# Kernel optimization log

Hardware: AMD Instinct MI355X
Metric: run time of the kernel (lower is better)

Reference implementation:

```python
import jax, jax.numpy as jnp
import numpy as np

LMAX, MMAX = 6, 2
N_NODES, N_EDGES = 10000, 80000
C_SPH = 32            # sphere_channels
D_DIST, H = 128, 64   # distance-basis width, radial hidden
MAX_ELEM = 90
RESCALE = 5.862
NUM_COEF_FULL = (LMAX + 1) ** 2   # 49
M0 = LMAX + 1                     # m=0 coefficient count = 7

def _orders():
    # reduced l-primary ordering: (l, m) for l in 0..LMAX, |m| <= min(l, MMAX)
    lp = [(l, m) for l in range(LMAX + 1) for m in range(-min(l, MMAX), min(l, MMAX) + 1)]
    # reduced m-primary ordering: m=0 block first, then (+m, -m) blocks, l ascending
    mp = [(l, 0) for l in range(LMAX + 1)]
    for m in range(1, MMAX + 1):
        mp += [(l, m) for l in range(m, LMAX + 1)]
        mp += [(l, -m) for l in range(m, LMAX + 1)]
    perm = np.array([mp.index(t) for t in lp])  # gather: m-primary -> l-primary
    full = [(l, m) for l in range(LMAX + 1) for m in range(-l, l + 1)]
    mask = np.array([i for i, (l, m) in enumerate(full) if abs(m) <= MMAX])
    return perm, mask

PERM_M2L, WIG_MASK = _orders()
M_ALL = len(PERM_M2L)  # 29


def setup_inputs() -> dict:
    key = jax.random.key(0)
    ks = jax.random.split(key, 10)
    return {
        "atomic_numbers": jax.random.randint(ks[0], (N_NODES,), 0, MAX_ELEM),
        "edge_index": jax.random.randint(ks[1], (2, N_EDGES), 0, N_NODES),
        "edge_distance": jax.random.normal(ks[2], (N_EDGES, D_DIST), jnp.float32),
        "wigner_inv": jax.random.normal(ks[3], (N_EDGES, NUM_COEF_FULL, NUM_COEF_FULL), jnp.float32) / np.float32(NUM_COEF_FULL) ** 0.5,
        "src_emb": jax.random.uniform(ks[4], (MAX_ELEM, H), jnp.float32, -0.001, 0.001),
        "tgt_emb": jax.random.uniform(ks[5], (MAX_ELEM, H), jnp.float32, -0.001, 0.001),
        "W1": jax.random.normal(ks[6], (D_DIST + 2 * H, H), jnp.float32) / np.float32(D_DIST + 2 * H) ** 0.5,
        "b1": jnp.zeros((H,), jnp.float32),
        "g1": jnp.ones((H,), jnp.float32),
        "be1": jnp.zeros((H,), jnp.float32),
        "W2": jax.random.normal(ks[7], (H, H), jnp.float32) / np.float32(H) ** 0.5,
        "b2": jnp.zeros((H,), jnp.float32),
        "g2": jnp.ones((H,), jnp.float32),
        "be2": jnp.zeros((H,), jnp.float32),
        "W3": jax.random.normal(ks[8], (H, M0 * C_SPH), jnp.float32) / np.float32(H) ** 0.5,
        "b3": jnp.zeros((M0 * C_SPH,), jnp.float32),
    }


def _ln(x, g, b):
    mu = jnp.mean(x, axis=-1, keepdims=True)
    var = jnp.var(x, axis=-1, keepdims=True)
    return (x - mu) * jax.lax.rsqrt(var + 1e-5) * g + b


def reference(atomic_numbers, edge_index, edge_distance, wigner_inv,
              src_emb, tgt_emb, W1, b1, g1, be1, W2, b2, g2, be2, W3, b3):
    # gather per-edge atom embeddings and build invariant edge scalars
    src = src_emb[atomic_numbers[edge_index[0]]]          # [E, H]
    tgt = tgt_emb[atomic_numbers[edge_index[1]]]          # [E, H]
    x = jnp.concatenate([edge_distance, src, tgt], axis=1)  # [E, D0+2H]
    # RadialFunction: Linear+LN+SiLU x2, final Linear -> m0 * C
    x = jax.nn.silu(_ln(x @ W1 + b1, g1, be1))
    x = jax.nn.silu(_ln(x @ W2 + b2, g2, be2))
    x = (x @ W3 + b3).reshape(-1, M0, C_SPH)              # [E, 7, C], m=0 coefficients
    # pad the m != 0 coefficients with zeros (m-primary layout, m=0 first)
    x = jnp.pad(x, ((0, 0), (0, M_ALL - M0), (0, 0)))     # [E, 29, C]
    # _l_primary: permute m-primary -> l-primary (to_m is a permutation matrix)
    x = x[:, PERM_M2L]                                    # [E, 29, C]
    # _rotate_inv: per-edge Wigner-D inverse, columns restricted to |m| <= mmax
    x = jnp.einsum('eij,ejc->eic', wigner_inv[:, :, WIG_MASK], x)  # [E, 49, C]
    # _reduce_edge: scatter-sum messages onto target nodes
    out = jax.ops.segment_sum(x, edge_index[1], num_segments=N_NODES)  # [N, 49, C]
    return out / RESCALE
```

## Files before the change

### kernel.cpp

```cpp
#include <hip/hip_runtime.h>
#include <hip/hip_bf16.h>
#include <stdint.h>

#define E_EDGES 80000
#define N_NODES 10000
#define HD      64
#define DDIST   128
#define NCOEF   49
#define W3OUT   224
#define WROW    2401
#define NELEM   90

typedef float  f32x4  __attribute__((ext_vector_type(4)));
typedef short  bf16x8 __attribute__((ext_vector_type(8)));
typedef unsigned int  uint_t;
typedef unsigned short ushort_t;

__device__ __forceinline__ ushort_t f2b(float f) {
    uint_t u = __builtin_bit_cast(uint_t, f);
    return (ushort_t)((u + 0x7FFFu + ((u >> 16) & 1u)) >> 16);
}
__device__ __forceinline__ uint_t pack2(float a, float b) {
    return (uint_t)f2b(a) | ((uint_t)f2b(b) << 16);
}

__global__ __launch_bounds__(256) void k_prep(
    const float* __restrict__ semb, const float* __restrict__ temb,
    const float* __restrict__ W1, const float* __restrict__ W2,
    const float* __restrict__ W3,
    float* __restrict__ sW1, float* __restrict__ tW1,
    ushort_t* __restrict__ W1T, ushort_t* __restrict__ W2T,
    ushort_t* __restrict__ W3T, int* __restrict__ cnt)
{
    const int gid = blockIdx.x * 256 + threadIdx.x;
    if (gid < NELEM * 64) {
        const int z = gid >> 6, n = gid & 63;
        float sa = 0.f, ta = 0.f;
        #pragma unroll 4
        for (int k = 0; k < 64; k++) {
            sa = fmaf(semb[z * 64 + k], W1[(128 + k) * 64 + n], sa);
            ta = fmaf(temb[z * 64 + k], W1[(192 + k) * 64 + n], ta);
        }
        sW1[z * 64 + n] = sa;
        tW1[z * 64 + n] = ta;
    }
    if (gid < 8192)  { const int n = gid >> 7, k = gid & 127; W1T[gid] = f2b(W1[k * 64 + n]); }
    if (gid < 4096)  { const int n = gid >> 6, k = gid & 63;  W2T[gid] = f2b(W2[k * 64 + n]); }
    if (gid < 14336) { const int n = gid >> 6, k = gid & 63;  W3T[gid] = f2b(W3[k * W3OUT + n]); }
    if (gid < N_NODES) cnt[gid] = 0;
}

__global__ __launch_bounds__(256, 3) void k_mlp(
    const int* __restrict__ an, const int* __restrict__ ei,
    const float* __restrict__ ed,
    const float* __restrict__ sW1, const float* __restrict__ tW1,
    const ushort_t* __restrict__ W1T, const ushort_t* __restrict__ W2T,
    const ushort_t* __restrict__ W3T,
    const float* __restrict__ b1, const float* __restrict__ g1,
    const float* __restrict__ be1,
    const float* __restrict__ b2, const float* __restrict__ g2,
    const float* __restrict__ be2,
    const float* __restrict__ b3, float* __restrict__ y3)
{
    __shared__ __align__(16) ushort_t Xs[64 * 128];
    __shared__ __align__(16) ushort_t Ws[64 * 128];
    __shared__ __align__(16) ushort_t Hs[64 * 64];
    __shared__ __align__(16) ushort_t H2s[64 * 64];

    const int tid  = threadIdx.x;
    const int wave = tid >> 6, lane = tid & 63;
    const int e0   = blockIdx.x * 64;
    const int mo   = wave * 16;
    const int cl   = lane & 15;
    const int kgr  = lane >> 4;

    {
        const int m = tid >> 2, q = tid & 3;
        const float4* ed4 = (const float4*)(ed + (size_t)(e0 + m) * DDIST);
        #pragma unroll
        for (int j = 0; j < 4; j++) {
            const int kb = q * 4 + j;
            const float4 f0 = ed4[kb * 2];
            const float4 f1 = ed4[kb * 2 + 1];
            uint4 p;
            p.x = pack2(f0.x, f0.y); p.y = pack2(f0.z, f0.w);
            p.z = pack2(f1.x, f1.y); p.w = pack2(f1.z, f1.w);
            *(uint4*)&Xs[m * 128 + ((kb ^ (m & 15)) * 8)] = p;
        }
    }
    {
        const uint4* src = (const uint4*)W1T;
        #pragma unroll
        for (int i = 0; i < 4; i++) {
            const int B = tid + i * 256;
            const int n = B >> 4, kb = B & 15;
            *(uint4*)&Ws[n * 128 + ((kb ^ (n & 15)) * 8)] = src[B];
        }
    }

    f32x4 acc[4];
    {
        const int er0 = e0 + mo + kgr * 4;
        const int4 s4 = *(const int4*)&ei[er0];
        const int4 t4 = *(const int4*)&ei[E_EDGES + er0];
        const int zs0 = an[s4.x], zs1 = an[s4.y], zs2 = an[s4.z], zs3 = an[s4.w];
        const int zt0 = an[t4.x], zt1 = an[t4.y], zt2 = an[t4.z], zt3 = an[t4.w];
        #pragma unroll
        for (int nf = 0; nf < 4; nf++) {
            const int col = nf * 16 + cl;
            acc[nf][0] = sW1[zs0 * 64 + col] + tW1[zt0 * 64 + col];
            acc[nf][1] = sW1[zs1 * 64 + col] + tW1[zt1 * 64 + col];
            acc[nf][2] = sW1[zs2 * 64 + col] + tW1[zt2 * 64 + col];
            acc[nf][3] = sW1[zs3 * 64 + col] + tW1[zt3 * 64 + col];
        }
    }
    __syncthreads();

    {
        const int m = mo + cl;
        #pragma unroll
        for (int kc = 0; kc < 4; kc++) {
            const int kb = kc * 4 + kgr;
            const bf16x8 a = *(const bf16x8*)&Xs[m * 128 + ((kb ^ (m & 15)) * 8)];
            #pragma unroll
            for (int nf = 0; nf < 4; nf++) {
                const int n = nf * 16 + cl;
                const bf16x8 b = *(const bf16x8*)&Ws[n * 128 + ((kb ^ (n & 15)) * 8)];
                acc[nf] = __builtin_amdgcn_mfma_f32_16x16x32_bf16(a, b, acc[nf], 0, 0, 0);
            }
        }
    }

    {
        float b1v[4], g1v[4], e1v[4];
        #pragma unroll
        for (int nf = 0; nf < 4; nf++) {
            b1v[nf] = b1[nf * 16 + cl];
            g1v[nf] = g1[nf * 16 + cl];
            e1v[nf] = be1[nf * 16 + cl];
        }
        #pragma unroll
        for (int nf = 0; nf < 4; nf++)
            #pragma unroll
            for (int r = 0; r < 4; r++) acc[nf][r] += b1v[nf];
        #pragma unroll
        for (int r = 0; r < 4; r++) {
            float s = acc[0][r] + acc[1][r] + acc[2][r] + acc[3][r];
            float q = acc[0][r]*acc[0][r] + acc[1][r]*acc[1][r]
                    + acc[2][r]*acc[2][r] + acc[3][r]*acc[3][r];
            s += __shfl_xor(s, 1, 64); q += __shfl_xor(q, 1, 64);
            s += __shfl_xor(s, 2, 64); q += __shfl_xor(q, 2, 64);
            s += __shfl_xor(s, 4, 64); q += __shfl_xor(q, 4, 64);
            s += __shfl_xor(s, 8, 64); q += __shfl_xor(q, 8, 64);
            const float mu  = s * (1.f / 64.f);
            const float var = fmaxf(q * (1.f / 64.f) - mu * mu, 0.f);
            const float rstd = rsqrtf(var + 1e-5f);
            const int m_h = mo + kgr * 4 + r;
            #pragma unroll
            for (int nf = 0; nf < 4; nf++) {
                const float t = (acc[nf][r] - mu) * rstd * g1v[nf] + e1v[nf];
                const float h = t / (1.f + expf(-t));
                const int ch = nf * 16 + cl;
                Hs[m_h * 64 + (((ch >> 3) ^ (m_h & 7)) * 8) + (ch & 7)] = f2b(h);
            }
        }
    }
    __syncthreads();

    {
        const uint4* src = (const uint4*)W2T;
        #pragma unroll
        for (int i = 0; i < 2; i++) {
            const int B = tid + i * 256;
            const int n = B >> 3, kb = B & 7;
            *(uint4*)&Ws[n * 64 + ((kb ^ (n & 7)) * 8)] = src[B];
        }
    }
    __syncthreads();

    f32x4 acc2[4];
    {
        const f32x4 z = {0.f, 0.f, 0.f, 0.f};
        acc2[0] = z; acc2[1] = z; acc2[2] = z; acc2[3] = z;
        const int m = mo + cl;
        #pragma unroll
        for (int kc = 0; kc < 2; kc++) {
            const int kb = kc * 4 + kgr;
            const bf16x8 a = *(const bf16x8*)&Hs[m * 64 + ((kb ^ (m & 7)) * 8)];
            #pragma unroll
            for (int nf = 0; nf < 4; nf++) {
                const int n = nf * 16 + cl;
                const bf16x8 b = *(const bf16x8*)&Ws[n * 64 + ((kb ^ (n & 7)) * 8)];
                acc2[nf] = __builtin_amdgcn_mfma_f32_16x16x32_bf16(a, b, acc2[nf], 0, 0, 0);
            }
        }
    }

    {
        float b2v[4], g2v[4], e2v[4];
        #pragma unroll
        for (int nf = 0; nf < 4; nf++) {
            b2v[nf] = b2[nf * 16 + cl];
            g2v[nf] = g2[nf * 16 + cl];
            e2v[nf] = be2[nf * 16 + cl];
        }
        #pragma unroll
        for (int nf = 0; nf < 4; nf++)
            #pragma unroll
            for (int r = 0; r < 4; r++) acc2[nf][r] += b2v[nf];
        #pragma unroll
        for (int r = 0; r < 4; r++) {
            float s = acc2[0][r] + acc2[1][r] + acc2[2][r] + acc2[3][r];
            float q = acc2[0][r]*acc2[0][r] + acc2[1][r]*acc2[1][r]
                    + acc2[2][r]*acc2[2][r] + acc2[3][r]*acc2[3][r];
            s += __shfl_xor(s, 1, 64); q += __shfl_xor(q, 1, 64);
            s += __shfl_xor(s, 2, 64); q += __shfl_xor(q, 2, 64);
            s += __shfl_xor(s, 4, 64); q += __shfl_xor(q, 4, 64);
            s += __shfl_xor(s, 8, 64); q += __shfl_xor(q, 8, 64);
            const float mu  = s * (1.f / 64.f);
            const float var = fmaxf(q * (1.f / 64.f) - mu * mu, 0.f);
            const float rstd = rsqrtf(var + 1e-5f);
            const int m_h = mo + kgr * 4 + r;
            #pragma unroll
            for (int nf = 0; nf < 4; nf++) {
                const float t = (acc2[nf][r] - mu) * rstd * g2v[nf] + e2v[nf];
                const float h = t / (1.f + expf(-t));
                const int ch = nf * 16 + cl;
                H2s[m_h * 64 + (((ch >> 3) ^ (m_h & 7)) * 8) + (ch & 7)] = f2b(h);
            }
        }
    }
    __syncthreads();

    const int er0 = e0 + mo + kgr * 4;
    #pragma unroll
    for (int half = 0; half < 2; half++) {
        {
            const uint4* src = (const uint4*)W3T;
            #pragma unroll
            for (int i = 0; i < 4; i++) {
                const int B = tid + i * 256;
                if (B < 896) {
                    const int nn = B >> 3, kb = B & 7;
                    *(uint4*)&Ws[nn * 64 + ((kb ^ (nn & 7)) * 8)] = src[half * 896 + B];
                }
            }
        }
        __syncthreads();

        f32x4 acc3[7];
        {
            const f32x4 z = {0.f, 0.f, 0.f, 0.f};
            #pragma unroll
            for (int nf = 0; nf < 7; nf++) acc3[nf] = z;
        }
        const int m = mo + cl;
        #pragma unroll
        for (int kc = 0; kc < 2; kc++) {
            const int kb = kc * 4 + kgr;
            const bf16x8 a = *(const bf16x8*)&H2s[m * 64 + ((kb ^ (m & 7)) * 8)];
            #pragma unroll
            for (int nf = 0; nf < 7; nf++) {
                const int nn = nf * 16 + cl;
                const bf16x8 b = *(const bf16x8*)&Ws[nn * 64 + ((kb ^ (nn & 7)) * 8)];
                acc3[nf] = __builtin_amdgcn_mfma_f32_16x16x32_bf16(a, b, acc3[nf], 0, 0, 0);
            }
        }
        #pragma unroll
        for (int nf = 0; nf < 7; nf++) {
            const int ch = half * 112 + nf * 16 + cl;
            const float bv = b3[ch];
            #pragma unroll
            for (int r = 0; r < 4; r++)
                y3[(size_t)(er0 + r) * W3OUT + ch] =
                    (acc3[nf][r] + bv) * (1.0f / 5.862f);
        }
        __syncthreads();
    }
}

__global__ void k_count(const int* __restrict__ ei, int* __restrict__ cnt) {
    const int e = blockIdx.x * 256 + threadIdx.x;
    if (e < E_EDGES) atomicAdd(&cnt[ei[E_EDGES + e]], 1);
}

__global__ __launch_bounds__(1024) void k_scan(const int* __restrict__ cnt,
                                               int* __restrict__ offs,
                                               int* __restrict__ cursor) {
    __shared__ int wsum[16];
    __shared__ int carry_s;
    const int tid  = threadIdx.x;
    const int lane = tid & 63;
    const int wid  = tid >> 6;
    if (tid == 0) carry_s = 0;
    __syncthreads();
    for (int base = 0; base < N_NODES; base += 1024) {
        const int idx = base + tid;
        const int v = (idx < N_NODES) ? cnt[idx] : 0;
        int s = v;
        #pragma unroll
        for (int off = 1; off < 64; off <<= 1) {
            const int t = __shfl_up(s, off, 64);
            if (lane >= off) s += t;
        }
        if (lane == 63) wsum[wid] = s;
        __syncthreads();
        if (wid == 0) {
            const int t = (lane < 16) ? wsum[lane] : 0;
            int ss = t;
            #pragma unroll
            for (int off = 1; off < 16; off <<= 1) {
                const int u = __shfl_up(ss, off, 64);
                if (lane >= off) ss += u;
            }
            if (lane < 16) wsum[lane] = ss - t;
        }
        __syncthreads();
        const int carry = carry_s;
        const int excl = carry + wsum[wid] + s - v;
        if (idx < N_NODES) { offs[idx] = excl; cursor[idx] = excl; }
        __syncthreads();
        if (tid == 1023) carry_s = carry + wsum[15] + s;
    }
    __syncthreads();
    if (tid == 0) offs[N_NODES] = carry_s;
}

__global__ void k_scatter(const int* __restrict__ ei, int* __restrict__ cursor,
                          int* __restrict__ eids) {
    const int e = blockIdx.x * 256 + threadIdx.x;
    if (e < E_EDGES) {
        const int pos = atomicAdd(&cursor[ei[E_EDGES + e]], 1);
        eids[pos] = e;
    }
}

__global__ __launch_bounds__(256) void k_out(
    const float* __restrict__ wig, const float* __restrict__ y3,
    const int* __restrict__ offs, const int* __restrict__ eids,
    float* __restrict__ out)
{
    __shared__ __align__(16) float wl[4][2][400];
    __shared__ __align__(16) float yl[4][2][224];
    const int tid  = threadIdx.x;
    const int wave = tid >> 6;
    const int lane = tid & 63;
    const int n    = blockIdx.x * 4 + wave;
    const int c    = lane & 31;
    const int h    = lane >> 5;
    const int beg  = offs[n];
    const int end  = offs[n + 1];

    float acc[25];
    #pragma unroll
    for (int r = 0; r < 25; r++) acc[r] = 0.f;

    float gv[6];
    float4 yv;

    #define GATHER(E) do {                                                  \
        const float* __restrict__ wb_ = wig + (size_t)(E) * WROW;           \
        _Pragma("unroll")                                                   \
        for (int g = 0; g < 6; g++) {                                       \
            const int t = lane + 64 * g;                                    \
            if (t < 343) {                                                  \
                const int row = t / 7;                                      \
                const int l   = t - row * 7;                                \
                gv[g] = wb_[row * 49 + l * l + l];                          \
            }                                                               \
        }                                                                   \
        if (lane < 56)                                                      \
            yv = ((const float4*)(y3 + (size_t)(E) * W3OUT))[lane];         \
    } while (0)

    #define COMMIT(B) do {                                                  \
        _Pragma("unroll")                                                   \
        for (int g = 0; g < 6; g++) {                                       \
            const int t = lane + 64 * g;                                    \
            if (t < 343) {                                                  \
                const int row = t / 7;                                      \
                const int l   = t - row * 7;                                \
                wl[wave][B][row * 8 + l] = gv[g];                           \
            }                                                               \
        }                                                                   \
        if (lane < 56) ((float4*)yl[wave][B])[lane] = yv;                   \
    } while (0)

    if (beg < end) {
        GATHER(eids[beg]);
        COMMIT(0);
    }

    int cur = 0;
    for (int ie = beg; ie < end; ie++) {
        if (ie + 1 < end) GATHER(eids[ie + 1]);
        asm volatile("s_waitcnt lgkmcnt(0)" ::: "memory");
        __builtin_amdgcn_sched_barrier(0);

        float yr[7];
        #pragma unroll
        for (int l = 0; l < 7; l++) yr[l] = yl[wave][cur][l * 32 + c];
        #pragma unroll
        for (int r = 0; r < 25; r++) {
            const int i = 2 * r + h;
            if (i < NCOEF) {
                const float4 wa = *(const float4*)(&wl[wave][cur][i * 8]);
                const float4 wb = *(const float4*)(&wl[wave][cur][i * 8 + 4]);
                acc[r] += wa.x * yr[0] + wa.y * yr[1] + wa.z * yr[2] + wa.w * yr[3]
                        + wb.x * yr[4] + wb.y * yr[5] + wb.z * yr[6];
            }
        }
        if (ie + 1 < end) COMMIT(cur ^ 1);
        cur ^= 1;
    }

    #pragma unroll
    for (int r = 0; r < 25; r++) {
        const int i = 2 * r + h;
        if (i < NCOEF)
            out[(size_t)n * (NCOEF * 32) + i * 32 + c] = acc[r];
    }
}

extern "C" void kernel_launch(void* const* d_in, const int* in_sizes, int n_in,
                              void* d_out, int out_size, void* d_ws, size_t ws_size,
                              hipStream_t stream)
{
    const int*   an   = (const int*)  d_in[0];
    const int*   ei   = (const int*)  d_in[1];
    const float* ed   = (const float*)d_in[2];
    const float* wig  = (const float*)d_in[3];
    const float* semb = (const float*)d_in[4];
    const float* temb = (const float*)d_in[5];
    const float* W1   = (const float*)d_in[6];
    const float* b1   = (const float*)d_in[7];
    const float* g1   = (const float*)d_in[8];
    const float* be1  = (const float*)d_in[9];
    const float* W2   = (const float*)d_in[10];
    const float* b2   = (const float*)d_in[11];
    const float* g2   = (const float*)d_in[12];
    const float* be2  = (const float*)d_in[13];
    const float* W3   = (const float*)d_in[14];
    const float* b3   = (const float*)d_in[15];
    float* out = (float*)d_out;

    uintptr_t p = (uintptr_t)d_ws;
    #define ALLOC(ptr, type, count) \
        p = (p + 15) & ~(uintptr_t)15; type* ptr = (type*)p; p += sizeof(type) * (count)
    ALLOC(y3,     float,    (size_t)E_EDGES * W3OUT);
    ALLOC(cnt,    int,      N_NODES);
    ALLOC(offs,   int,      N_NODES + 1);
    ALLOC(cursor, int,      N_NODES);
    ALLOC(eids,   int,      E_EDGES);
    ALLOC(sW1,    float,    NELEM * HD);
    ALLOC(tW1,    float,    NELEM * HD);
    ALLOC(W1T,    ushort_t, 64 * 128);
    ALLOC(W2T,    ushort_t, 64 * 64);
    ALLOC(W3T,    ushort_t, 224 * 64);
    #undef ALLOC
    if (p - (uintptr_t)d_ws > ws_size) return;

    k_prep<<<56, 256, 0, stream>>>(semb, temb, W1, W2, W3,
                                   sW1, tW1, W1T, W2T, W3T, cnt);
    k_mlp<<<E_EDGES / 64, 256, 0, stream>>>(an, ei, ed, sW1, tW1,
                                            W1T, W2T, W3T,
                                            b1, g1, be1, b2, g2, be2,
                                            b3, y3);
    k_count<<<(E_EDGES + 255) / 256, 256, 0, stream>>>(ei, cnt);
    k_scan<<<1, 1024, 0, stream>>>(cnt, offs, cursor);
    k_scatter<<<(E_EDGES + 255) / 256, 256, 0, stream>>>(ei, cursor, eids);
    k_out<<<N_NODES / 4, 256, 0, stream>>>(wig, y3, offs, eids, out);
}
```

Baseline: 279.9 us.

## Store radial MLP output as bf16 and deepen gather prefetch in k_out

```diff
diff --git a/kernel.cpp b/kernel.cpp
--- a/kernel.cpp
+++ b/kernel.cpp
@@ -22,6 +22,9 @@
 }
 __device__ __forceinline__ uint_t pack2(float a, float b) {
     return (uint_t)f2b(a) | ((uint_t)f2b(b) << 16);
+}
+__device__ __forceinline__ float b2f(uint_t v) {
+    return __builtin_bit_cast(float, v << 16);
 }
 
 __global__ __launch_bounds__(256) void k_prep(
@@ -60,7 +63,7 @@
     const float* __restrict__ be1,
     const float* __restrict__ b2, const float* __restrict__ g2,
     const float* __restrict__ be2,
-    const float* __restrict__ b3, float* __restrict__ y3)
+    const float* __restrict__ b3, ushort_t* __restrict__ y3)
 {
     __shared__ __align__(16) ushort_t Xs[64 * 128];
     __shared__ __align__(16) ushort_t Ws[64 * 128];
@@ -273,7 +276,7 @@
             #pragma unroll
             for (int r = 0; r < 4; r++)
                 y3[(size_t)(er0 + r) * W3OUT + ch] =
-                    (acc3[nf][r] + bv) * (1.0f / 5.862f);
+                    f2b((acc3[nf][r] + bv) * (1.0f / 5.862f));
         }
         __syncthreads();
     }
@@ -336,7 +339,7 @@
 }
 
 __global__ __launch_bounds__(256) void k_out(
-    const float* __restrict__ wig, const float* __restrict__ y3,
+    const float* __restrict__ wig, const ushort_t* __restrict__ y3,
     const int* __restrict__ offs, const int* __restrict__ eids,
     float* __restrict__ out)
 {
@@ -355,10 +358,10 @@
     #pragma unroll
     for (int r = 0; r < 25; r++) acc[r] = 0.f;
 
-    float gv[6];
-    float4 yv;
-
-    #define GATHER(E) do {                                                  \
+    float gvA[6], gvB[6];
+    uint2 yvA, yvB;
+
+    #define GATHER(S, E) do {                                               \
         const float* __restrict__ wb_ = wig + (size_t)(E) * WROW;           \
         _Pragma("unroll")                                                   \
         for (int g = 0; g < 6; g++) {                                       \
@@ -366,52 +369,70 @@
             if (t < 343) {                                                  \
                 const int row = t / 7;                                      \
                 const int l   = t - row * 7;                                \
-                gv[g] = wb_[row * 49 + l * l + l];                          \
+                gv##S[g] = wb_[row * 49 + l * l + l];                       \
             }                                                               \
         }                                                                   \
         if (lane < 56)                                                      \
-            yv = ((const float4*)(y3 + (size_t)(E) * W3OUT))[lane];         \
+            yv##S = ((const uint2*)(y3 + (size_t)(E) * W3OUT))[lane];       \
     } while (0)
 
-    #define COMMIT(B) do {                                                  \
+    #define COMMIT(S, B) do {                                               \
         _Pragma("unroll")                                                   \
         for (int g = 0; g < 6; g++) {                                       \
             const int t = lane + 64 * g;                                    \
             if (t < 343) {                                                  \
                 const int row = t / 7;                                      \
                 const int l   = t - row * 7;                                \
-                wl[wave][B][row * 8 + l] = gv[g];                           \
+                wl[wave][B][row * 8 + l] = gv##S[g];                        \
             }                                                               \
         }                                                                   \
-        if (lane < 56) ((float4*)yl[wave][B])[lane] = yv;                   \
+        if (lane < 56) {                                                    \
+            float4 yf;                                                      \
+            yf.x = b2f(yv##S.x & 0xffffu);                                  \
+            yf.y = b2f(yv##S.x >> 16);                                      \
+            yf.z = b2f(yv##S.y & 0xffffu);                                  \
+            yf.w = b2f(yv##S.y >> 16);                                      \
+            ((float4*)yl[wave][B])[lane] = yf;                              \
+        }                                                                   \
     } while (0)
 
-    if (beg < end) {
-        GATHER(eids[beg]);
-        COMMIT(0);
-    }
-
-    int cur = 0;
-    for (int ie = beg; ie < end; ie++) {
-        if (ie + 1 < end) GATHER(eids[ie + 1]);
-        asm volatile("s_waitcnt lgkmcnt(0)" ::: "memory");
-        __builtin_amdgcn_sched_barrier(0);
-
-        float yr[7];
-        #pragma unroll
-        for (int l = 0; l < 7; l++) yr[l] = yl[wave][cur][l * 32 + c];
-        #pragma unroll
-        for (int r = 0; r < 25; r++) {
-            const int i = 2 * r + h;
-            if (i < NCOEF) {
-                const float4 wa = *(const float4*)(&wl[wave][cur][i * 8]);
-                const float4 wb = *(const float4*)(&wl[wave][cur][i * 8 + 4]);
-                acc[r] += wa.x * yr[0] + wa.y * yr[1] + wa.z * yr[2] + wa.w * yr[3]
-                        + wb.x * yr[4] + wb.y * yr[5] + wb.z * yr[6];
-            }
-        }
-        if (ie + 1 < end) COMMIT(cur ^ 1);
-        cur ^= 1;
+    #define FENCE() do {                                                    \
+        asm volatile("s_waitcnt lgkmcnt(0)" ::: "memory");                  \
+        __builtin_amdgcn_sched_barrier(0);                                  \
+    } while (0)
+
+    #define COMPUTE(B) do {                                                 \
+        float yr[7];                                                        \
+        _Pragma("unroll")                                                   \
+        for (int l = 0; l < 7; l++) yr[l] = yl[wave][B][l * 32 + c];        \
+        _Pragma("unroll")                                                   \
+        for (int r = 0; r < 25; r++) {                                      \
+            const int i = 2 * r + h;                                        \
+            if (i < NCOEF) {                                                \
+                const float4 wa = *(const float4*)(&wl[wave][B][i * 8]);    \
+                const float4 wb = *(const float4*)(&wl[wave][B][i * 8 + 4]);\
+                acc[r] += wa.x * yr[0] + wa.y * yr[1] + wa.z * yr[2]        \
+                        + wa.w * yr[3] + wb.x * yr[4] + wb.y * yr[5]        \
+                        + wb.z * yr[6];                                     \
+            }                                                               \
+        }                                                                   \
+    } while (0)
+
+    if (beg < end)     GATHER(A, eids[beg]);
+    if (beg + 1 < end) GATHER(B, eids[beg + 1]);
+    if (beg < end)     COMMIT(A, 0);
+
+    for (int ie = beg; ie < end; ie += 2) {
+        if (ie + 2 < end) GATHER(A, eids[ie + 2]);
+        FENCE();
+        COMPUTE(0);
+        if (ie + 1 < end) COMMIT(B, 1);
+        if (ie + 1 < end) {
+            if (ie + 3 < end) GATHER(B, eids[ie + 3]);
+            FENCE();
+            COMPUTE(1);
+            if (ie + 2 < end) COMMIT(A, 0);
+        }
     }
 
     #pragma unroll
@@ -447,7 +468,7 @@
     uintptr_t p = (uintptr_t)d_ws;
     #define ALLOC(ptr, type, count) \
         p = (p + 15) & ~(uintptr_t)15; type* ptr = (type*)p; p += sizeof(type) * (count)
-    ALLOC(y3,     float,    (size_t)E_EDGES * W3OUT);
+    ALLOC(y3,     ushort_t, (size_t)E_EDGES * W3OUT);
     ALLOC(cnt,    int,      N_NODES);
     ALLOC(offs,   int,      N_NODES + 1);
     ALLOC(cursor, int,      N_NODES);
```

New measurement: 265.5 us. -5.2%, faster.
